# Kernel optimization log

Hardware: AMD Instinct MI355X
Metric: run time of the kernel (lower is better)

The kernel has to match this reference:

```python
import jax, jax.numpy as jnp
import numpy as np

TEMPERATURE = 0.07


def setup_inputs() -> dict:
    key = jax.random.key(0)
    k1, k2 = jax.random.split(key)
    B, D = 4096, 512
    emb1 = jax.random.normal(k1, (B, D), dtype=jnp.float32)
    emb2 = jax.random.normal(k2, (B, D), dtype=jnp.float32)
    # module assumes L2-normalised embeddings
    emb1 = emb1 / jnp.linalg.norm(emb1, axis=-1, keepdims=True)
    emb2 = emb2 / jnp.linalg.norm(emb2, axis=-1, keepdims=True)
    return {"emb1": emb1, "emb2": emb2}


def reference(emb1, emb2):
    B = emb1.shape[0]
    emb = jnp.concatenate([emb1, emb2], axis=0)            # (2B, D)
    sim = jnp.einsum('id,jd->ij', emb, emb) / TEMPERATURE  # (2B, 2B)
    neg_inf = jnp.finfo(sim.dtype).min
    self_mask = jnp.eye(2 * B, dtype=bool)
    sim = jnp.where(self_mask, neg_inf, sim)
    labels = jnp.concatenate([jnp.arange(B, 2 * B), jnp.arange(B)])
    logp = jax.nn.log_softmax(sim, axis=-1)                # stable softmax CE
    nll = -jnp.take_along_axis(logp, labels[:, None], axis=-1)[:, 0]
    return jnp.mean(nll)
```

## Files before the change

kernel.cpp:

```cpp
#include <hip/hip_runtime.h>
#include <hip/hip_bf16.h>

#define B_    4096
#define D_    512
#define TB_   8192
#define BM    128
#define BK    128
#define NK    4
#define NTILE 64
#define NTRI  2080
#define INV_T 14.285714285714286f
#define SCL   (INV_T / 16129.0f)

typedef __attribute__((ext_vector_type(4))) int   v4i;

#define GLOAD_LDS16(gp, lp)                                                        \
  __builtin_amdgcn_global_load_lds((const __attribute__((address_space(1))) void*)(gp), \
                                   (__attribute__((address_space(3))) void*)(lp),  \
                                   16, 0, 0)

__global__ void ntx_prep(const float* __restrict__ a, const float* __restrict__ b,
                         char* __restrict__ E8, float* __restrict__ L) {
  int t = blockIdx.x * blockDim.x + threadIdx.x;
  int i = t * 16;
  const float* src = (i < B_ * D_) ? (a + i) : (b + (i - B_ * D_));
  v4i o;
#pragma unroll
  for (int g = 0; g < 4; ++g) {
    float4 v = ((const float4*)src)[g];
    int q0 = __float2int_rn(v.x * 127.0f) & 255;
    int q1 = __float2int_rn(v.y * 127.0f) & 255;
    int q2 = __float2int_rn(v.z * 127.0f) & 255;
    int q3 = __float2int_rn(v.w * 127.0f) & 255;
    o[g] = q0 | (q1 << 8) | (q2 << 16) | (q3 << 24);
  }
  ((v4i*)E8)[t] = o;
  if (t < TB_) L[t] = 0.0f;
}

__global__ __launch_bounds__(256, 4)
void ntx_sim(const char* __restrict__ E8, float* __restrict__ L,
             float* __restrict__ pos) {
  __shared__ __align__(16) char As[BM * BK];
  __shared__ __align__(16) char Bs[BM * BK];

  const int bid = blockIdx.x;
  const int t   = (bid & 7) * (NTRI / 8) + (bid >> 3);
  int ti = (int)((129.0f - sqrtf(16641.0f - 8.0f * (float)t)) * 0.5f);
  while (ti * (129 - ti) / 2 > t) --ti;
  while ((ti + 1) * (128 - ti) / 2 <= t) ++ti;
  const int tj = ti + (t - ti * (129 - ti) / 2);
  const int rowTile = ti * BM, colTile = tj * BM;
  const bool diag = (ti == tj);
  const bool posT = (tj == ti + B_ / BM);

  const int tid = threadIdx.x, lane = tid & 63, wave = tid >> 6;
  const int wr = wave >> 1, wc = wave & 1;
  const int llo = lane & 15, lhi = lane >> 4;

  unsigned offA[4], offB[4], ldsOf[4];
#pragma unroll
  for (int r = 0; r < 4; ++r) {
    int ch = r * 256 + tid, row = ch >> 3;
    int sc = ((ch & 7) ^ (row & 7)) << 4;
    offA[r]  = (unsigned)(rowTile + row) * D_ + sc;
    offB[r]  = (unsigned)(colTile + row) * D_ + sc;
    ldsOf[r] = (unsigned)ch * 16;
  }
  unsigned fA[2][4], fB[2][4];
#pragma unroll
  for (int ks = 0; ks < 2; ++ks)
#pragma unroll
    for (int m = 0; m < 4; ++m) {
      int chc = ks * 4 + lhi;
      int ra  = wr * 64 + m * 16 + llo;
      fA[ks][m] = (unsigned)(ra * BK + (((unsigned)chc ^ (ra & 7)) << 4));
      int rb  = wc * 64 + m * 16 + llo;
      fB[ks][m] = (unsigned)(rb * BK + (((unsigned)chc ^ (rb & 7)) << 4));
    }

  v4i acc[4][4] = {};

  for (int kt = 0; kt < NK; ++kt) {
    const unsigned kb = (unsigned)kt * BK;
#pragma unroll
    for (int r = 0; r < 4; ++r) GLOAD_LDS16(E8 + offA[r] + kb, &As[ldsOf[r]]);
#pragma unroll
    for (int r = 0; r < 4; ++r) GLOAD_LDS16(E8 + offB[r] + kb, &Bs[ldsOf[r]]);
    __syncthreads();
#pragma unroll
    for (int ks = 0; ks < 2; ++ks) {
      v4i af[4], bf[4];
#pragma unroll
      for (int m = 0; m < 4; ++m) {
        af[m] = *(const v4i*)&As[fA[ks][m]];
        bf[m] = *(const v4i*)&Bs[fB[ks][m]];
      }
#pragma unroll
      for (int m = 0; m < 4; ++m)
#pragma unroll
        for (int n = 0; n < 4; ++n)
          acc[m][n] = __builtin_amdgcn_mfma_i32_16x16x64_i8(af[m], bf[n],
                                                            acc[m][n], 0, 0, 0);
    }
    __syncthreads();
  }

  float cs[4] = {0.f, 0.f, 0.f, 0.f};
#pragma unroll
  for (int m = 0; m < 4; ++m) {
    float rs[4] = {0.f, 0.f, 0.f, 0.f};
#pragma unroll
    for (int n = 0; n < 4; ++n) {
      int gc = colTile + wc * 64 + n * 16 + llo;
#pragma unroll
      for (int jj = 0; jj < 4; ++jj) {
        int gr = rowTile + wr * 64 + m * 16 + lhi * 4 + jj;
        float s = (float)acc[m][n][jj] * SCL;
        if (posT && gc - gr == B_) pos[gr] = s;
        float e = __expf(s);
        e = (diag && gr == gc) ? 0.0f : e;
        rs[jj] += e;
        cs[n]  += e;
      }
    }
#pragma unroll
    for (int jj = 0; jj < 4; ++jj) {
      float v = rs[jj];
      v += __shfl_xor(v, 1);
      v += __shfl_xor(v, 2);
      v += __shfl_xor(v, 4);
      v += __shfl_xor(v, 8);
      if (llo == 0) {
        int gr = rowTile + wr * 64 + m * 16 + lhi * 4 + jj;
        atomicAdd(&L[gr], v);
      }
    }
  }
  if (!diag) {
#pragma unroll
    for (int n = 0; n < 4; ++n) {
      float v = cs[n];
      v += __shfl_xor(v, 16);
      v += __shfl_xor(v, 32);
      if (lhi == 0) {
        int gc = colTile + wc * 64 + n * 16 + llo;
        atomicAdd(&L[gc], v);
      }
    }
  }
}

__global__ void ntx_fin(const float* __restrict__ L, const float* __restrict__ pos,
                        float* __restrict__ out) {
  int tid = threadIdx.x;
  float s = 0.f;
#pragma unroll
  for (int k = 0; k < TB_ / 256; ++k) {
    int r = k * 256 + tid;
    s += __logf(L[r]) - pos[r & (B_ - 1)];
  }
#pragma unroll
  for (int off = 1; off < 64; off <<= 1) s += __shfl_xor(s, off);
  __shared__ float sm[4];
  if ((tid & 63) == 0) sm[tid >> 6] = s;
  __syncthreads();
  if (tid == 0) out[0] = (sm[0] + sm[1] + sm[2] + sm[3]) * (1.0f / TB_);
}

extern "C" void kernel_launch(void* const* d_in, const int* in_sizes, int n_in,
                              void* d_out, int out_size, void* d_ws, size_t ws_size,
                              hipStream_t stream) {
  const float* e1 = (const float*)d_in[0];
  const float* e2 = (const float*)d_in[1];
  float* out = (float*)d_out;
  char* E8   = (char*)d_ws;
  float* L   = (float*)((char*)d_ws + (size_t)TB_ * D_);
  float* pos = L + TB_;

  ntx_prep<<<1024, 256, 0, stream>>>(e1, e2, E8, L);
  ntx_sim<<<NTRI, 256, 0, stream>>>(E8, L, pos);
  ntx_fin<<<1, 256, 0, stream>>>(L, pos, out);
}
```

Measured before the change: 61.65 us.

## Use single-wave 64x64 triangular tiles with in-wave prefetch and no block barriers

Shrinks the upper-triangular tile from 128 to 64 and gives each tile to one 64-thread wave, which removes __syncthreads and lets the next K slice be staged into LDS while the second half of the current slice's MFMAs runs. It also replaces expf with exp2f on a pre-scaled constant. The cost is more global traffic, since each tile reuses less data, plus four times as many blocks and atomics, and a smaller per-block LDS footprint. Overwriting LDS only after lgkmcnt(0) inside one wave keeps the single-buffer reuse safe.

```diff
diff --git a/kernel.cpp b/kernel.cpp
--- a/kernel.cpp
+++ b/kernel.cpp
@@ -4,15 +4,16 @@
 #define B_    4096
 #define D_    512
 #define TB_   8192
-#define BM    128
+#define BM    64
 #define BK    128
 #define NK    4
-#define NTILE 64
-#define NTRI  2080
+#define NTILE 128
+#define NTRI  8256
 #define INV_T 14.285714285714286f
 #define SCL   (INV_T / 16129.0f)
+#define SCL2  (SCL * 1.4426950408889634f)
 
-typedef __attribute__((ext_vector_type(4))) int   v4i;
+typedef __attribute__((ext_vector_type(4))) int v4i;
 
 #define GLOAD_LDS16(gp, lp)                                                        \
   __builtin_amdgcn_global_load_lds((const __attribute__((address_space(1))) void*)(gp), \
@@ -38,7 +39,13 @@
   if (t < TB_) L[t] = 0.0f;
 }
 
-__global__ __launch_bounds__(256, 4)
+#define STG(kt)                                                                    \
+  do { _Pragma("unroll") for (int r = 0; r < 8; ++r) {                             \
+         GLOAD_LDS16(E8 + offA[r] + (kt) * BK, &As[r * 1024 + lane * 16]);         \
+         GLOAD_LDS16(E8 + offB[r] + (kt) * BK, &Bs[r * 1024 + lane * 16]);         \
+       } } while (0)
+
+__global__ __launch_bounds__(64, 3)
 void ntx_sim(const char* __restrict__ E8, float* __restrict__ L,
              float* __restrict__ pos) {
   __shared__ __align__(16) char As[BM * BK];
@@ -46,26 +53,24 @@
 
   const int bid = blockIdx.x;
   const int t   = (bid & 7) * (NTRI / 8) + (bid >> 3);
-  int ti = (int)((129.0f - sqrtf(16641.0f - 8.0f * (float)t)) * 0.5f);
-  while (ti * (129 - ti) / 2 > t) --ti;
-  while ((ti + 1) * (128 - ti) / 2 <= t) ++ti;
-  const int tj = ti + (t - ti * (129 - ti) / 2);
+  int ti = (int)((257.0f - sqrtf(66049.0f - 8.0f * (float)t)) * 0.5f);
+  while (ti * (257 - ti) / 2 > t) --ti;
+  while ((ti + 1) * (256 - ti) / 2 <= t) ++ti;
+  const int tj = ti + (t - ti * (257 - ti) / 2);
   const int rowTile = ti * BM, colTile = tj * BM;
   const bool diag = (ti == tj);
   const bool posT = (tj == ti + B_ / BM);
 
-  const int tid = threadIdx.x, lane = tid & 63, wave = tid >> 6;
-  const int wr = wave >> 1, wc = wave & 1;
+  const int lane = threadIdx.x & 63;
   const int llo = lane & 15, lhi = lane >> 4;
 
-  unsigned offA[4], offB[4], ldsOf[4];
+  unsigned offA[8], offB[8];
 #pragma unroll
-  for (int r = 0; r < 4; ++r) {
-    int ch = r * 256 + tid, row = ch >> 3;
+  for (int r = 0; r < 8; ++r) {
+    int ch = r * 64 + lane, row = ch >> 3;
     int sc = ((ch & 7) ^ (row & 7)) << 4;
-    offA[r]  = (unsigned)(rowTile + row) * D_ + sc;
-    offB[r]  = (unsigned)(colTile + row) * D_ + sc;
-    ldsOf[r] = (unsigned)ch * 16;
+    offA[r] = (unsigned)(rowTile + row) * D_ + sc;
+    offB[r] = (unsigned)(colTile + row) * D_ + sc;
   }
   unsigned fA[2][4], fB[2][4];
 #pragma unroll
@@ -73,37 +78,44 @@
 #pragma unroll
     for (int m = 0; m < 4; ++m) {
       int chc = ks * 4 + lhi;
-      int ra  = wr * 64 + m * 16 + llo;
+      int ra  = m * 16 + llo;
       fA[ks][m] = (unsigned)(ra * BK + (((unsigned)chc ^ (ra & 7)) << 4));
-      int rb  = wc * 64 + m * 16 + llo;
+      int rb  = m * 16 + llo;
       fB[ks][m] = (unsigned)(rb * BK + (((unsigned)chc ^ (rb & 7)) << 4));
     }
 
   v4i acc[4][4] = {};
 
+  STG(0);
+#pragma unroll
   for (int kt = 0; kt < NK; ++kt) {
-    const unsigned kb = (unsigned)kt * BK;
+    asm volatile("s_waitcnt vmcnt(0)" ::: "memory");
+    v4i af[4], bf[4];
 #pragma unroll
-    for (int r = 0; r < 4; ++r) GLOAD_LDS16(E8 + offA[r] + kb, &As[ldsOf[r]]);
+    for (int m = 0; m < 4; ++m) {
+      af[m] = *(const v4i*)&As[fA[0][m]];
+      bf[m] = *(const v4i*)&Bs[fB[0][m]];
+    }
 #pragma unroll
-    for (int r = 0; r < 4; ++r) GLOAD_LDS16(E8 + offB[r] + kb, &Bs[ldsOf[r]]);
-    __syncthreads();
+    for (int m = 0; m < 4; ++m)
 #pragma unroll
-    for (int ks = 0; ks < 2; ++ks) {
-      v4i af[4], bf[4];
+      for (int n = 0; n < 4; ++n)
+        acc[m][n] = __builtin_amdgcn_mfma_i32_16x16x64_i8(af[m], bf[n],
+                                                          acc[m][n], 0, 0, 0);
+    v4i ag[4], bg[4];
 #pragma unroll
-      for (int m = 0; m < 4; ++m) {
-        af[m] = *(const v4i*)&As[fA[ks][m]];
-        bf[m] = *(const v4i*)&Bs[fB[ks][m]];
-      }
+    for (int m = 0; m < 4; ++m) {
+      ag[m] = *(const v4i*)&As[fA[1][m]];
+      bg[m] = *(const v4i*)&Bs[fB[1][m]];
+    }
+    asm volatile("s_waitcnt lgkmcnt(0)" ::: "memory");
+    if (kt + 1 < NK) STG(kt + 1);
 #pragma unroll
-      for (int m = 0; m < 4; ++m)
+    for (int m = 0; m < 4; ++m)
 #pragma unroll
-        for (int n = 0; n < 4; ++n)
-          acc[m][n] = __builtin_amdgcn_mfma_i32_16x16x64_i8(af[m], bf[n],
-                                                            acc[m][n], 0, 0, 0);
-    }
-    __syncthreads();
+      for (int n = 0; n < 4; ++n)
+        acc[m][n] = __builtin_amdgcn_mfma_i32_16x16x64_i8(ag[m], bg[n],
+                                                          acc[m][n], 0, 0, 0);
   }
 
   float cs[4] = {0.f, 0.f, 0.f, 0.f};
@@ -112,13 +124,12 @@
     float rs[4] = {0.f, 0.f, 0.f, 0.f};
 #pragma unroll
     for (int n = 0; n < 4; ++n) {
-      int gc = colTile + wc * 64 + n * 16 + llo;
+      int gc = colTile + n * 16 + llo;
 #pragma unroll
       for (int jj = 0; jj < 4; ++jj) {
-        int gr = rowTile + wr * 64 + m * 16 + lhi * 4 + jj;
-        float s = (float)acc[m][n][jj] * SCL;
-        if (posT && gc - gr == B_) pos[gr] = s;
-        float e = __expf(s);
+        int gr = rowTile + m * 16 + lhi * 4 + jj;
+        if (posT && gc - gr == B_) pos[gr] = (float)acc[m][n][jj] * SCL;
+        float e = exp2f((float)acc[m][n][jj] * SCL2);
         e = (diag && gr == gc) ? 0.0f : e;
         rs[jj] += e;
         cs[n]  += e;
@@ -132,7 +143,7 @@
       v += __shfl_xor(v, 4);
       v += __shfl_xor(v, 8);
       if (llo == 0) {
-        int gr = rowTile + wr * 64 + m * 16 + lhi * 4 + jj;
+        int gr = rowTile + m * 16 + lhi * 4 + jj;
         atomicAdd(&L[gr], v);
       }
     }
@@ -144,7 +155,7 @@
       v += __shfl_xor(v, 16);
       v += __shfl_xor(v, 32);
       if (lhi == 0) {
-        int gc = colTile + wc * 64 + n * 16 + llo;
+        int gc = colTile + n * 16 + llo;
         atomicAdd(&L[gc], v);
       }
     }
@@ -179,6 +190,6 @@
   float* pos = L + TB_;
 
   ntx_prep<<<1024, 256, 0, stream>>>(e1, e2, E8, L);
-  ntx_sim<<<NTRI, 256, 0, stream>>>(E8, L, pos);
+  ntx_sim<<<NTRI, 64, 0, stream>>>(E8, L, pos);
   ntx_fin<<<1, 256, 0, stream>>>(L, pos, out);
 }
```

Result: slower. 89.23 us (+44.7%).
